# Optimization experiments

Hardware: AMD Instinct MI355X
Metric: run time of the kernel (lower is better)

The kernel has to match this reference:

```python
import jax, jax.numpy as jnp
import numpy as np

B, S, D, H = 4, 2048, 1024, 16
DQKV = max(1, D // H)  # 64


def setup_inputs() -> dict:
    key = jax.random.key(0)
    ks = jax.random.split(key, 12)
    std = 1.0 / np.sqrt(D)
    inp = {
        "query": jax.random.normal(ks[0], (B, S, D), dtype=jnp.float32),
        "key": jax.random.normal(ks[1], (B, S, D), dtype=jnp.float32),
        "value": jax.random.normal(ks[2], (B, S, D), dtype=jnp.float32),
        # per-head projection weights, stacked over heads: [H, DQKV, D] (torch Linear layout [out,in])
        "wq": jax.random.uniform(ks[3], (H, DQKV, D), jnp.float32, -std, std),
        "bq": jax.random.uniform(ks[4], (H, DQKV), jnp.float32, -std, std),
        "wk": jax.random.uniform(ks[5], (H, DQKV, D), jnp.float32, -std, std),
        "bk": jax.random.uniform(ks[6], (H, DQKV), jnp.float32, -std, std),
        "wv": jax.random.uniform(ks[7], (H, DQKV, D), jnp.float32, -std, std),
        "bv": jax.random.uniform(ks[8], (H, DQKV), jnp.float32, -std, std),
        # output projection: [D, H*DQKV]
        "wo": jax.random.uniform(ks[9], (D, H * DQKV), jnp.float32, -1.0 / np.sqrt(H * DQKV), 1.0 / np.sqrt(H * DQKV)),
        "bo": jax.random.uniform(ks[10], (D,), jnp.float32, -1.0 / np.sqrt(H * DQKV), 1.0 / np.sqrt(H * DQKV)),
    }
    return inp


def reference(query, key, value, wq, bq, wk, bk, wv, bv, wo, bo):
    # Per-head linear projections (batched over heads): [B, H, S, DQKV]
    Q = jnp.einsum("bsd,hed->bhse", query, wq) + bq[None, :, None, :]
    K = jnp.einsum("bsd,hed->bhse", key, wk) + bk[None, :, None, :]
    V = jnp.einsum("bsd,hed->bhse", value, wv) + bv[None, :, None, :]
    scale = jnp.asarray(DQKV, Q.dtype) ** 0.5
    # Full N x N attention scores per head (matches naive bmm+softmax+bmm)
    scores = jnp.einsum("bhse,bhte->bhst", Q, K) / scale
    attn = jax.nn.softmax(scores, axis=-1)
    ctx = jnp.einsum("bhst,bhte->bhse", attn, V)  # [B, H, S, DQKV]
    # Concat over heads in head-major order: [B, S, H*DQKV]
    concat = jnp.transpose(ctx, (0, 2, 1, 3)).reshape(ctx.shape[0], ctx.shape[2], H * DQKV)
    return jnp.einsum("bsf,df->bsd", concat, wo) + bo
```

## Files before the change

### kernel.cpp

```cpp
#include <hip/hip_runtime.h>
#include <stdint.h>
#include <stddef.h>


typedef __attribute__((ext_vector_type(8))) short short8;
typedef __attribute__((ext_vector_type(4))) float f32x4;

#if __has_builtin(__builtin_amdgcn_exp2f)
#define EXP2F __builtin_amdgcn_exp2f
#else
#define EXP2F exp2f
#endif
#if __has_builtin(__builtin_amdgcn_rcpf)
#define RCPF __builtin_amdgcn_rcpf
#else
#define RCPF(x) (1.0f / (x))
#endif

__device__ __forceinline__ uint16_t f2bf(float f) {
  uint32_t u = __builtin_bit_cast(uint32_t, f);
  u += 0x7FFFu + ((u >> 16) & 1u);
  return (uint16_t)(u >> 16);
}

__device__ __forceinline__ void gld16(const void* g, void* l) {
  __builtin_amdgcn_global_load_lds((const __attribute__((address_space(1))) void*)g,
                                   (__attribute__((address_space(3))) void*)l, 16, 0, 0);
}

__global__ __launch_bounds__(256) void cast3(const float* __restrict__ s0, const float* __restrict__ s1,
                                             const float* __restrict__ s2, uint16_t* __restrict__ d0,
                                             uint16_t* __restrict__ d1, uint16_t* __restrict__ d2,
                                             int n4) {
  const int z = blockIdx.y;
  const float* s = z == 0 ? s0 : (z == 1 ? s1 : s2);
  uint16_t* d = z == 0 ? d0 : (z == 1 ? d1 : d2);
  int i = blockIdx.x * 256 + threadIdx.x;
  if (i >= n4) return;
  float4 v = ((const float4*)s)[i];
  ushort4 o;
  o.x = f2bf(v.x); o.y = f2bf(v.y); o.z = f2bf(v.z); o.w = f2bf(v.w);
  ((ushort4*)d)[i] = o;
}

__global__ __launch_bounds__(256) void cast4(const float* __restrict__ s0, const float* __restrict__ s1,
                                             const float* __restrict__ s2, const float* __restrict__ s3,
                                             uint16_t* __restrict__ d0, uint16_t* __restrict__ d1,
                                             uint16_t* __restrict__ d2, uint16_t* __restrict__ d3,
                                             int n4) {
  const int z = blockIdx.y;
  const float* s = z == 0 ? s0 : (z == 1 ? s1 : (z == 2 ? s2 : s3));
  uint16_t* d = z == 0 ? d0 : (z == 1 ? d1 : (z == 2 ? d2 : d3));
  int i = blockIdx.x * 256 + threadIdx.x;
  if (i >= n4) return;
  float4 v = ((const float4*)s)[i];
  ushort4 o;
  o.x = f2bf(v.x); o.y = f2bf(v.y); o.z = f2bf(v.z); o.w = f2bf(v.w);
  ((ushort4*)d)[i] = o;
}

template <int MODE>
__global__ __launch_bounds__(256) void gemm_bt(const uint16_t* __restrict__ A,
                                               const uint16_t* __restrict__ Bw,
                                               const float* __restrict__ bias,
                                               void* __restrict__ Cout, float oscale) {
  constexpr int K = 1024;
  __shared__ __attribute__((aligned(16))) uint16_t As[128 * 32];
  __shared__ __attribute__((aligned(16))) uint16_t Bs[128 * 32];
  const int tid = threadIdx.x;
  const int w = tid >> 6, l = tid & 63;
  const int ln = l & 15, quad = l >> 4;
  const int m0 = blockIdx.y * 128, n0 = blockIdx.x * 128;
  const int wm = (w >> 1) * 64, wn = (w & 1) * 64;

  f32x4 acc[4][4] = {};

  const uint16_t* Ag[2];
  const uint16_t* Bg[2];
  int lofs[2];
#pragma unroll
  for (int c = 0; c < 2; ++c) {
    int chunk = w * 128 + c * 64 + l;
    int r = chunk >> 2, cc = chunk & 3;
    Ag[c] = A + (size_t)(m0 + r) * K + cc * 8;
    Bg[c] = Bw + (size_t)(n0 + r) * K + cc * 8;
    lofs[c] = (w * 128 + c * 64) * 8;
  }

  for (int k0 = 0; k0 < K; k0 += 32) {
    __syncthreads();
#pragma unroll
    for (int c = 0; c < 2; ++c) {
      gld16(Ag[c] + k0, As + lofs[c]);
      gld16(Bg[c] + k0, Bs + lofs[c]);
    }
    __syncthreads();
    short8 a[4], b[4];
#pragma unroll
    for (int mt = 0; mt < 4; ++mt)
      a[mt] = *(const short8*)(As + (wm + mt * 16 + ln) * 32 + quad * 8);
#pragma unroll
    for (int nt = 0; nt < 4; ++nt)
      b[nt] = *(const short8*)(Bs + (wn + nt * 16 + ln) * 32 + quad * 8);
#pragma unroll
    for (int mt = 0; mt < 4; ++mt)
#pragma unroll
      for (int nt = 0; nt < 4; ++nt)
        acc[mt][nt] = __builtin_amdgcn_mfma_f32_16x16x32_bf16(a[mt], b[nt], acc[mt][nt], 0, 0, 0);
  }

#pragma unroll
  for (int nt = 0; nt < 4; ++nt) {
    const int col = n0 + wn + nt * 16 + ln;
    const float bv = bias[col];
#pragma unroll
    for (int mt = 0; mt < 4; ++mt) {
#pragma unroll
      for (int i = 0; i < 4; ++i) {
        const int row = m0 + wm + mt * 16 + quad * 4 + i;
        const float v = acc[mt][nt][i] + bv;
        if (MODE == 0) {
          const int b_ = row >> 11, s = row & 2047, h = col >> 6, e = col & 63;
          ((uint16_t*)Cout)[(size_t)(b_ * 16 + h) * 131072 + s * 64 + e] = f2bf(v * oscale);
        } else if (MODE == 1) {
          const int b_ = row >> 11, s = row & 2047, h = col >> 6, e = col & 63;
          ((uint16_t*)Cout)[(size_t)(b_ * 16 + h) * 131072 + e * 2048 + s] = f2bf(v);
        } else {
          ((float*)Cout)[(size_t)row * 1024 + col] = v;
        }
      }
    }
  }
}

__global__ __launch_bounds__(256) void attn(const uint16_t* __restrict__ Qb,
                                            const uint16_t* __restrict__ Kb,
                                            const uint16_t* __restrict__ Vtb,
                                            uint16_t* __restrict__ Ctx) {
  __shared__ __attribute__((aligned(16))) uint16_t Ks[128 * 64];
  __shared__ __attribute__((aligned(16))) uint16_t Vs[64 * 128];
  __shared__ __attribute__((aligned(16))) uint16_t Ps[4 * 16 * 136];
  const int tid = threadIdx.x;
  const int w = tid >> 6, l = tid & 63;
  const int ln = l & 15, quad = l >> 4;
  const int bh = blockIdx.y;
  const int b = bh >> 4, h = bh & 15;
  const int q0 = blockIdx.x * 64;
  const uint16_t* Qh = Qb + (size_t)bh * 131072;
  const uint16_t* Kh = Kb + (size_t)bh * 131072;
  const uint16_t* Vth = Vtb + (size_t)bh * 131072;

  short8 qf[2];
#pragma unroll
  for (int ks = 0; ks < 2; ++ks)
    qf[ks] = *(const short8*)(Qh + (size_t)(q0 + w * 16 + ln) * 64 + ks * 32 + quad * 8);

  short8 ones;
#pragma unroll
  for (int j = 0; j < 8; ++j) ones[j] = (short)0x3F80;

  f32x4 oacc[4] = {};
  f32x4 lacc = {};

  for (int t0 = 0; t0 < 2048; t0 += 128) {
    __syncthreads();
#pragma unroll
    for (int c = 0; c < 4; ++c) {
      const int f = w * 256 + c * 64 + l;
      const int t = f >> 3, cp = f & 7, g = (cp - t) & 7;
      gld16(Kh + (size_t)(t0 + t) * 64 + g * 8, Ks + (w * 256 + c * 64) * 8);
      const int e = f >> 4, cp2 = f & 15, g2 = (cp2 - e) & 15;
      gld16(Vth + (size_t)e * 2048 + t0 + g2 * 8, Vs + (w * 256 + c * 64) * 8);
    }
    __syncthreads();

    f32x4 sacc[8] = {};
#pragma unroll
    for (int nt = 0; nt < 8; ++nt) {
      const int t = nt * 16 + ln;
#pragma unroll
      for (int ks = 0; ks < 2; ++ks) {
        const int c = ks * 4 + quad;
        const short8 kf = *(const short8*)(Ks + (t * 8 + ((c + t) & 7)) * 8);
        sacc[nt] = __builtin_amdgcn_mfma_f32_16x16x32_bf16(qf[ks], kf, sacc[nt], 0, 0, 0);
      }
    }

#pragma unroll
    for (int nt = 0; nt < 8; ++nt) {
#pragma unroll
      for (int i = 0; i < 4; ++i) {
        const float p = EXP2F(sacc[nt][i]);
        const uint32_t u = __builtin_bit_cast(uint32_t, p) + 0x8000u;
        Ps[w * 2176 + (quad * 4 + i) * 136 + nt * 16 + ln] = (uint16_t)(u >> 16);
      }
    }

#pragma unroll
    for (int ks = 0; ks < 4; ++ks) {
      const short8 pf = *(const short8*)(Ps + w * 2176 + ln * 136 + ks * 32 + quad * 8);
      lacc = __builtin_amdgcn_mfma_f32_16x16x32_bf16(pf, ones, lacc, 0, 0, 0);
#pragma unroll
      for (int nt = 0; nt < 4; ++nt) {
        const int e = nt * 16 + ln;
        const int c = ks * 4 + quad;
        const short8 vf = *(const short8*)(Vs + (e * 16 + ((c + e) & 15)) * 8);
        oacc[nt] = __builtin_amdgcn_mfma_f32_16x16x32_bf16(pf, vf, oacc[nt], 0, 0, 0);
      }
    }
  }

  float inv[4];
#pragma unroll
  for (int i = 0; i < 4; ++i) inv[i] = RCPF(lacc[i]);
#pragma unroll
  for (int nt = 0; nt < 4; ++nt) {
#pragma unroll
    for (int i = 0; i < 4; ++i) {
      const float v = oacc[nt][i] * inv[i];
      const int s = q0 + w * 16 + quad * 4 + i;
      Ctx[(size_t)(b * 2048 + s) * 1024 + h * 64 + nt * 16 + ln] = f2bf(v);
    }
  }
}

extern "C" void kernel_launch(void* const* d_in, const int* in_sizes, int n_in,
                              void* d_out, int out_size, void* d_ws, size_t ws_size,
                              hipStream_t stream) {
  const float* q = (const float*)d_in[0];
  const float* k = (const float*)d_in[1];
  const float* v = (const float*)d_in[2];
  const float* wq = (const float*)d_in[3];
  const float* bq = (const float*)d_in[4];
  const float* wk = (const float*)d_in[5];
  const float* bk = (const float*)d_in[6];
  const float* wv = (const float*)d_in[7];
  const float* bv = (const float*)d_in[8];
  const float* wo = (const float*)d_in[9];
  const float* bo = (const float*)d_in[10];
  float* out = (float*)d_out;

  uint16_t* ws = (uint16_t*)d_ws;
  uint16_t* Xq = ws;
  uint16_t* Xk = Xq + 8388608;
  uint16_t* Xv = Xk + 8388608;
  uint16_t* Wq = Xv + 8388608;
  uint16_t* Wk = Wq + 1048576;
  uint16_t* Wv = Wk + 1048576;
  uint16_t* Wo = Wv + 1048576;
  uint16_t* Qb = Wo + 1048576;
  uint16_t* Kb = Qb + 8388608;
  uint16_t* Vtb = Xk;
  uint16_t* Ctx = Xq;

  cast3<<<dim3(8192, 3), 256, 0, stream>>>(q, k, v, Xq, Xk, Xv, 2097152);
  cast4<<<dim3(1024, 4), 256, 0, stream>>>(wq, wk, wv, wo, Wq, Wk, Wv, Wo, 262144);

  const float qscale = 0.125f * 1.4426950408889634f;
  dim3 ggrid(8, 64);
  gemm_bt<0><<<ggrid, 256, 0, stream>>>(Xq, Wq, bq, Qb, qscale);
  gemm_bt<0><<<ggrid, 256, 0, stream>>>(Xk, Wk, bk, Kb, 1.0f);
  gemm_bt<1><<<ggrid, 256, 0, stream>>>(Xv, Wv, bv, Vtb, 1.0f);

  attn<<<dim3(32, 64), 256, 0, stream>>>(Qb, Kb, Vtb, Ctx);

  gemm_bt<2><<<ggrid, 256, 0, stream>>>(Ctx, Wo, bo, out, 1.0f);
}
```

Baseline: 406.1 us.

## Fuse QKV projection GEMMs into one launch and double attention query tile

Merges the three Q/K/V projection GEMMs into a single launch over a z dimension when the workspace is large enough to hold a separate V buffer, so the three GEMMs can share the GPU at once instead of running back-to-back. The attention kernel now processes 128 queries per block, with two 16-row sub-tiles per wave, so each K/V tile loaded to shared memory is reused twice as much. The cost is higher register and LDS use per block and half as many attention blocks, which may reduce occupancy. The fused path relies on a larger workspace and falls back to three launches otherwise.

```diff
diff --git a/kernel.cpp b/kernel.cpp
--- a/kernel.cpp
+++ b/kernel.cpp
@@ -59,21 +59,15 @@
   ((ushort4*)d)[i] = o;
 }
 
-template <int MODE>
-__global__ __launch_bounds__(256) void gemm_bt(const uint16_t* __restrict__ A,
-                                               const uint16_t* __restrict__ Bw,
-                                               const float* __restrict__ bias,
-                                               void* __restrict__ Cout, float oscale) {
+__device__ __forceinline__ void gemm_core(const uint16_t* __restrict__ A,
+                                          const uint16_t* __restrict__ Bw,
+                                          uint16_t* As, uint16_t* Bs,
+                                          f32x4 acc[4][4], int m0, int n0) {
   constexpr int K = 1024;
-  __shared__ __attribute__((aligned(16))) uint16_t As[128 * 32];
-  __shared__ __attribute__((aligned(16))) uint16_t Bs[128 * 32];
   const int tid = threadIdx.x;
   const int w = tid >> 6, l = tid & 63;
   const int ln = l & 15, quad = l >> 4;
-  const int m0 = blockIdx.y * 128, n0 = blockIdx.x * 128;
   const int wm = (w >> 1) * 64, wn = (w & 1) * 64;
-
-  f32x4 acc[4][4] = {};
 
   const uint16_t* Ag[2];
   const uint16_t* Bg[2];
@@ -108,28 +102,77 @@
       for (int nt = 0; nt < 4; ++nt)
         acc[mt][nt] = __builtin_amdgcn_mfma_f32_16x16x32_bf16(a[mt], b[nt], acc[mt][nt], 0, 0, 0);
   }
-
+}
+
+__global__ __launch_bounds__(256) void gemm_qkv(const uint16_t* __restrict__ Xq, const uint16_t* __restrict__ Xk,
+                                                const uint16_t* __restrict__ Xv, const uint16_t* __restrict__ Wq,
+                                                const uint16_t* __restrict__ Wk, const uint16_t* __restrict__ Wv,
+                                                const float* __restrict__ bq, const float* __restrict__ bk,
+                                                const float* __restrict__ bv, uint16_t* __restrict__ Qb,
+                                                uint16_t* __restrict__ Kb, uint16_t* __restrict__ Vtb,
+                                                float qscale, int zbase) {
+  __shared__ __attribute__((aligned(16))) uint16_t As[128 * 32];
+  __shared__ __attribute__((aligned(16))) uint16_t Bs[128 * 32];
+  const int z = blockIdx.z + zbase;
+  const uint16_t* A = z == 0 ? Xq : (z == 1 ? Xk : Xv);
+  const uint16_t* Bw = z == 0 ? Wq : (z == 1 ? Wk : Wv);
+  const float* bias = z == 0 ? bq : (z == 1 ? bk : bv);
+  uint16_t* Cout = z == 0 ? Qb : (z == 1 ? Kb : Vtb);
+  const float scale = z == 0 ? qscale : 1.0f;
+
+  const int m0 = blockIdx.y * 128, n0 = blockIdx.x * 128;
+  f32x4 acc[4][4] = {};
+  gemm_core(A, Bw, As, Bs, acc, m0, n0);
+
+  const int tid = threadIdx.x;
+  const int w = tid >> 6, l = tid & 63;
+  const int ln = l & 15, quad = l >> 4;
+  const int wm = (w >> 1) * 64, wn = (w & 1) * 64;
 #pragma unroll
   for (int nt = 0; nt < 4; ++nt) {
     const int col = n0 + wn + nt * 16 + ln;
-    const float bv = bias[col];
+    const float bv_ = bias[col];
+    const int h = col >> 6, e = col & 63;
 #pragma unroll
     for (int mt = 0; mt < 4; ++mt) {
 #pragma unroll
       for (int i = 0; i < 4; ++i) {
         const int row = m0 + wm + mt * 16 + quad * 4 + i;
-        const float v = acc[mt][nt][i] + bv;
-        if (MODE == 0) {
-          const int b_ = row >> 11, s = row & 2047, h = col >> 6, e = col & 63;
-          ((uint16_t*)Cout)[(size_t)(b_ * 16 + h) * 131072 + s * 64 + e] = f2bf(v * oscale);
-        } else if (MODE == 1) {
-          const int b_ = row >> 11, s = row & 2047, h = col >> 6, e = col & 63;
-          ((uint16_t*)Cout)[(size_t)(b_ * 16 + h) * 131072 + e * 2048 + s] = f2bf(v);
+        const int b_ = row >> 11, s = row & 2047;
+        const float v = (acc[mt][nt][i] + bv_) * scale;
+        if (z != 2) {
+          Cout[(size_t)(b_ * 16 + h) * 131072 + s * 64 + e] = f2bf(v);
         } else {
-          ((float*)Cout)[(size_t)row * 1024 + col] = v;
+          Cout[(size_t)(b_ * 16 + h) * 131072 + e * 2048 + s] = f2bf(v);
         }
       }
     }
+  }
+}
+
+__global__ __launch_bounds__(256) void gemm_out(const uint16_t* __restrict__ A, const uint16_t* __restrict__ Bw,
+                                                const float* __restrict__ bias, float* __restrict__ Cout) {
+  __shared__ __attribute__((aligned(16))) uint16_t As[128 * 32];
+  __shared__ __attribute__((aligned(16))) uint16_t Bs[128 * 32];
+  const int m0 = blockIdx.y * 128, n0 = blockIdx.x * 128;
+  f32x4 acc[4][4] = {};
+  gemm_core(A, Bw, As, Bs, acc, m0, n0);
+
+  const int tid = threadIdx.x;
+  const int w = tid >> 6, l = tid & 63;
+  const int ln = l & 15, quad = l >> 4;
+  const int wm = (w >> 1) * 64, wn = (w & 1) * 64;
+#pragma unroll
+  for (int nt = 0; nt < 4; ++nt) {
+    const int col = n0 + wn + nt * 16 + ln;
+    const float bv_ = bias[col];
+#pragma unroll
+    for (int mt = 0; mt < 4; ++mt)
+#pragma unroll
+      for (int i = 0; i < 4; ++i) {
+        const int row = m0 + wm + mt * 16 + quad * 4 + i;
+        Cout[(size_t)row * 1024 + col] = acc[mt][nt][i] + bv_;
+      }
   }
 }
 
@@ -139,28 +182,30 @@
                                             uint16_t* __restrict__ Ctx) {
   __shared__ __attribute__((aligned(16))) uint16_t Ks[128 * 64];
   __shared__ __attribute__((aligned(16))) uint16_t Vs[64 * 128];
-  __shared__ __attribute__((aligned(16))) uint16_t Ps[4 * 16 * 136];
+  __shared__ __attribute__((aligned(16))) uint16_t Ps[4 * 2 * 16 * 136];
   const int tid = threadIdx.x;
   const int w = tid >> 6, l = tid & 63;
   const int ln = l & 15, quad = l >> 4;
   const int bh = blockIdx.y;
   const int b = bh >> 4, h = bh & 15;
-  const int q0 = blockIdx.x * 64;
+  const int q0 = blockIdx.x * 128;
   const uint16_t* Qh = Qb + (size_t)bh * 131072;
   const uint16_t* Kh = Kb + (size_t)bh * 131072;
   const uint16_t* Vth = Vtb + (size_t)bh * 131072;
 
-  short8 qf[2];
-#pragma unroll
-  for (int ks = 0; ks < 2; ++ks)
-    qf[ks] = *(const short8*)(Qh + (size_t)(q0 + w * 16 + ln) * 64 + ks * 32 + quad * 8);
+  short8 qf[2][2];
+#pragma unroll
+  for (int sub = 0; sub < 2; ++sub)
+#pragma unroll
+    for (int ks = 0; ks < 2; ++ks)
+      qf[sub][ks] = *(const short8*)(Qh + (size_t)(q0 + w * 32 + sub * 16 + ln) * 64 + ks * 32 + quad * 8);
 
   short8 ones;
 #pragma unroll
   for (int j = 0; j < 8; ++j) ones[j] = (short)0x3F80;
 
-  f32x4 oacc[4] = {};
-  f32x4 lacc = {};
+  f32x4 oacc[2][4] = {};
+  f32x4 lacc[2] = {};
 
   for (int t0 = 0; t0 < 2048; t0 += 128) {
     __syncthreads();
@@ -174,7 +219,7 @@
     }
     __syncthreads();
 
-    f32x4 sacc[8] = {};
+    f32x4 sacc[2][8] = {};
 #pragma unroll
     for (int nt = 0; nt < 8; ++nt) {
       const int t = nt * 16 + ln;
@@ -182,45 +227,52 @@
       for (int ks = 0; ks < 2; ++ks) {
         const int c = ks * 4 + quad;
         const short8 kf = *(const short8*)(Ks + (t * 8 + ((c + t) & 7)) * 8);
-        sacc[nt] = __builtin_amdgcn_mfma_f32_16x16x32_bf16(qf[ks], kf, sacc[nt], 0, 0, 0);
-      }
-    }
-
-#pragma unroll
-    for (int nt = 0; nt < 8; ++nt) {
-#pragma unroll
-      for (int i = 0; i < 4; ++i) {
-        const float p = EXP2F(sacc[nt][i]);
-        const uint32_t u = __builtin_bit_cast(uint32_t, p) + 0x8000u;
-        Ps[w * 2176 + (quad * 4 + i) * 136 + nt * 16 + ln] = (uint16_t)(u >> 16);
-      }
-    }
+        sacc[0][nt] = __builtin_amdgcn_mfma_f32_16x16x32_bf16(qf[0][ks], kf, sacc[0][nt], 0, 0, 0);
+        sacc[1][nt] = __builtin_amdgcn_mfma_f32_16x16x32_bf16(qf[1][ks], kf, sacc[1][nt], 0, 0, 0);
+      }
+    }
+
+#pragma unroll
+    for (int sub = 0; sub < 2; ++sub)
+#pragma unroll
+      for (int nt = 0; nt < 8; ++nt)
+#pragma unroll
+        for (int i = 0; i < 4; ++i) {
+          const float p = EXP2F(sacc[sub][nt][i]);
+          const uint32_t u = __builtin_bit_cast(uint32_t, p) + 0x8000u;
+          Ps[w * 4352 + sub * 2176 + (quad * 4 + i) * 136 + nt * 16 + ln] = (uint16_t)(u >> 16);
+        }
 
 #pragma unroll
     for (int ks = 0; ks < 4; ++ks) {
-      const short8 pf = *(const short8*)(Ps + w * 2176 + ln * 136 + ks * 32 + quad * 8);
-      lacc = __builtin_amdgcn_mfma_f32_16x16x32_bf16(pf, ones, lacc, 0, 0, 0);
+      const short8 pf0 = *(const short8*)(Ps + w * 4352 + ln * 136 + ks * 32 + quad * 8);
+      const short8 pf1 = *(const short8*)(Ps + w * 4352 + 2176 + ln * 136 + ks * 32 + quad * 8);
+      lacc[0] = __builtin_amdgcn_mfma_f32_16x16x32_bf16(pf0, ones, lacc[0], 0, 0, 0);
+      lacc[1] = __builtin_amdgcn_mfma_f32_16x16x32_bf16(pf1, ones, lacc[1], 0, 0, 0);
 #pragma unroll
       for (int nt = 0; nt < 4; ++nt) {
         const int e = nt * 16 + ln;
         const int c = ks * 4 + quad;
         const short8 vf = *(const short8*)(Vs + (e * 16 + ((c + e) & 15)) * 8);
-        oacc[nt] = __builtin_amdgcn_mfma_f32_16x16x32_bf16(pf, vf, oacc[nt], 0, 0, 0);
-      }
-    }
-  }
-
-  float inv[4];
-#pragma unroll
-  for (int i = 0; i < 4; ++i) inv[i] = RCPF(lacc[i]);
-#pragma unroll
-  for (int nt = 0; nt < 4; ++nt) {
-#pragma unroll
-    for (int i = 0; i < 4; ++i) {
-      const float v = oacc[nt][i] * inv[i];
-      const int s = q0 + w * 16 + quad * 4 + i;
-      Ctx[(size_t)(b * 2048 + s) * 1024 + h * 64 + nt * 16 + ln] = f2bf(v);
-    }
+        oacc[0][nt] = __builtin_amdgcn_mfma_f32_16x16x32_bf16(pf0, vf, oacc[0][nt], 0, 0, 0);
+        oacc[1][nt] = __builtin_amdgcn_mfma_f32_16x16x32_bf16(pf1, vf, oacc[1][nt], 0, 0, 0);
+      }
+    }
+  }
+
+#pragma unroll
+  for (int sub = 0; sub < 2; ++sub) {
+    float inv[4];
+#pragma unroll
+    for (int i = 0; i < 4; ++i) inv[i] = RCPF(lacc[sub][i]);
+#pragma unroll
+    for (int nt = 0; nt < 4; ++nt)
+#pragma unroll
+      for (int i = 0; i < 4; ++i) {
+        const float v = oacc[sub][nt][i] * inv[i];
+        const int s = q0 + w * 32 + sub * 16 + quad * 4 + i;
+        Ctx[(size_t)(b * 2048 + s) * 1024 + h * 64 + nt * 16 + ln] = f2bf(v);
+      }
   }
 }
 
@@ -250,19 +302,29 @@
   uint16_t* Wo = Wv + 1048576;
   uint16_t* Qb = Wo + 1048576;
   uint16_t* Kb = Qb + 8388608;
-  uint16_t* Vtb = Xk;
   uint16_t* Ctx = Xq;
+
+  const size_t fused_elems = 46137344u + 8388608u;
+  const bool fused = ws_size >= fused_elems * sizeof(uint16_t);
+  uint16_t* Vtb = fused ? (Kb + 8388608) : Xk;
 
   cast3<<<dim3(8192, 3), 256, 0, stream>>>(q, k, v, Xq, Xk, Xv, 2097152);
   cast4<<<dim3(1024, 4), 256, 0, stream>>>(wq, wk, wv, wo, Wq, Wk, Wv, Wo, 262144);
 
   const float qscale = 0.125f * 1.4426950408889634f;
-  dim3 ggrid(8, 64);
-  gemm_bt<0><<<ggrid, 256, 0, stream>>>(Xq, Wq, bq, Qb, qscale);
-  gemm_bt<0><<<ggrid, 256, 0, stream>>>(Xk, Wk, bk, Kb, 1.0f);
-  gemm_bt<1><<<ggrid, 256, 0, stream>>>(Xv, Wv, bv, Vtb, 1.0f);
-
-  attn<<<dim3(32, 64), 256, 0, stream>>>(Qb, Kb, Vtb, Ctx);
-
-  gemm_bt<2><<<ggrid, 256, 0, stream>>>(Ctx, Wo, bo, out, 1.0f);
-}
+  if (fused) {
+    gemm_qkv<<<dim3(8, 64, 3), 256, 0, stream>>>(Xq, Xk, Xv, Wq, Wk, Wv, bq, bk, bv,
+                                                 Qb, Kb, Vtb, qscale, 0);
+  } else {
+    gemm_qkv<<<dim3(8, 64, 1), 256, 0, stream>>>(Xq, Xk, Xv, Wq, Wk, Wv, bq, bk, bv,
+                                                 Qb, Kb, Vtb, qscale, 0);
+    gemm_qkv<<<dim3(8, 64, 1), 256, 0, stream>>>(Xq, Xk, Xv, Wq, Wk, Wv, bq, bk, bv,
+                                                 Qb, Kb, Vtb, qscale, 1);
+    gemm_qkv<<<dim3(8, 64, 1), 256, 0, stream>>>(Xq, Xk, Xv, Wq, Wk, Wv, bq, bk, bv,
+                                                 Qb, Kb, Vtb, qscale, 2);
+  }
+
+  attn<<<dim3(16, 64), 256, 0, stream>>>(Qb, Kb, Vtb, Ctx);
+
+  gemm_out<<<dim3(8, 64), 256, 0, stream>>>(Ctx, Wo, bo, out);
+}
```

Measured after the change: 390.6 us. 3.8% less time.
